# Optimization experiments

Measured on AMD Instinct MI355X. Metric: run time of the kernel, lower is better.

## Reference

```python
import jax, jax.numpy as jnp
import numpy as np

N_V = 100000   # vertices
N_E = 20000    # hyperedges
N_PAIRS = 1600000  # incidence pairs
F = 128
H = 128
EPS = 1e-5


def setup_inputs() -> dict:
    key = jax.random.key(0)
    k1, k2, k3, k4 = jax.random.split(key, 4)
    X = jax.random.normal(k1, (N_V, F), dtype=jnp.float32)
    vertex_ids = jax.random.randint(k2, (N_PAIRS,), 0, N_V, dtype=jnp.int32)
    edge_ids = jax.random.randint(k3, (N_PAIRS,), 0, N_E, dtype=jnp.int32)
    W = jax.random.normal(k4, (F, H), dtype=jnp.float32) * (1.0 / np.sqrt(F))
    b = jnp.zeros((H,), dtype=jnp.float32)
    gamma = jnp.ones((H,), dtype=jnp.float32)
    beta = jnp.zeros((H,), dtype=jnp.float32)
    return {"X": X, "vertex_ids": vertex_ids, "edge_ids": edge_ids,
            "W": W, "b": b, "gamma": gamma, "beta": beta}


def _segment_mean(vals, ids, num_segments):
    s = jax.ops.segment_sum(vals, ids, num_segments=num_segments)
    cnt = jax.ops.segment_sum(jnp.ones((ids.shape[0], 1), vals.dtype), ids,
                              num_segments=num_segments)
    return s / jnp.maximum(cnt, 1.0)


def reference(X, vertex_ids, edge_ids, W, b, gamma, beta):
    # linear: theta
    h = X @ W + b                                    # [N_V, H]
    # batchnorm (batch statistics, as in training mode)
    mu = jnp.mean(h, axis=0)
    var = jnp.var(h, axis=0)
    h = (h - mu) * jax.lax.rsqrt(var + EPS) * gamma + beta
    # hypergraph v2v mean: vertex -> hyperedge mean, then hyperedge -> vertex mean
    Xe = _segment_mean(h[vertex_ids], edge_ids, N_E)   # [N_E, H]
    Xv = _segment_mean(Xe[edge_ids], vertex_ids, N_V)  # [N_V, H]
    # activation (ReLU); dropout is identity in eval
    return jax.nn.relu(Xv)
```

## Files before the change

kernel.cpp:

```cpp
#include <hip/hip_runtime.h>
#include <hip/hip_bf16.h>

#define N_V 100000
#define N_E 20000
#define N_P 1600000
#define FDIM 128
#define HDIM 128
#define BN_EPS 1e-5f

#define SORT_C 4096
#define SORT_BLOCKS ((N_P + SORT_C - 1) / SORT_C)
#define NB_E 313
#define EB_SHIFT 6
#define EB_REGION 9216
#define EB_SORT 5888
#define NB_V 391
#define VB_SHIFT 8
#define VB_REGION 8192
#define VB_SORT 4608
#define SENTINEL 0xFFFFFFFFu

#define EIDX_CAP 192
#define VIDX_CAP 64

#define GEMM_BLOCKS 625
#define WT_STRIDE 136
#define BN_BLOCKS 400
#define BN_RPB 250

typedef __attribute__((ext_vector_type(8))) short short8;
typedef __attribute__((ext_vector_type(4))) float floatx4;

__device__ __forceinline__ float bf_lo(unsigned u) {
    return __uint_as_float(u << 16);
}
__device__ __forceinline__ float bf_hi(unsigned u) {
    return __uint_as_float(u & 0xffff0000u);
}
__device__ __forceinline__ unsigned short f2bf(float f) {
    unsigned u = __float_as_uint(f);
    return (unsigned short)((u + 0x7fffu + ((u >> 16) & 1u)) >> 16);
}

__device__ __forceinline__ void acc4(float* s, const uint2& u) {
    s[0] += bf_lo(u.x); s[1] += bf_hi(u.x);
    s[2] += bf_lo(u.y); s[3] += bf_hi(u.y);
}

__device__ __forceinline__ void acc8(float* s, const uint4& u) {
    s[0] += bf_lo(u.x); s[1] += bf_hi(u.x);
    s[2] += bf_lo(u.y); s[3] += bf_hi(u.y);
    s[4] += bf_lo(u.z); s[5] += bf_hi(u.z);
    s[6] += bf_lo(u.w); s[7] += bf_hi(u.w);
}

union SmemK1 {
    struct {
        unsigned short WTs[FDIM * WT_STRIDE];
    } g;
    struct {
        unsigned stage[SORT_C];
        int hist[NB_E], cur[NB_E], offs[NB_E], gbase[NB_E];
        int partial[256];
    } se;
    struct {
        unsigned stage[SORT_C];
        int hist[NB_V], cur[NB_V], offs[NB_V], gbase[NB_V];
        int partial[256];
    } sv;
};

union SmemBnCsr {
    struct {
        unsigned B[EB_SORT];
        int hist[256];
        int offs[257];
        int cur[256];
    } c;
    struct {
        float ls[128], lss[128];
    } b;
};

__device__ void gemm_body(int bid, unsigned short* WTs,
                          const float* __restrict__ X,
                          const float* __restrict__ W,
                          const float* __restrict__ bias,
                          unsigned* __restrict__ h_u) {
    const int t = threadIdx.x;
    for (int idx = t; idx < FDIM * HDIM; idx += 256) {
        const int k = idx >> 7, m = idx & 127;
        WTs[m * WT_STRIDE + k] = f2bf(W[idx]);
    }
    __syncthreads();

    const int wave = t >> 6, lane = t & 63;
    const int quad = lane >> 4, sub = lane & 15;
    const int nstrips = N_V / 16;

    for (int s = bid * 4 + wave; s < nstrips; s += GEMM_BLOCKS * 4) {
        const int row0 = s * 16;
        short8 xf[4];
        const float* xp = X + (size_t)(row0 + sub) * FDIM + quad * 8;
        #pragma unroll
        for (int kt = 0; kt < 4; ++kt) {
            const float4 a = *(const float4*)(xp + kt * 32);
            const float4 b2 = *(const float4*)(xp + kt * 32 + 4);
            short8 f;
            f[0] = (short)f2bf(a.x);  f[1] = (short)f2bf(a.y);
            f[2] = (short)f2bf(a.z);  f[3] = (short)f2bf(a.w);
            f[4] = (short)f2bf(b2.x); f[5] = (short)f2bf(b2.y);
            f[6] = (short)f2bf(b2.z); f[7] = (short)f2bf(b2.w);
            xf[kt] = f;
        }
        #pragma unroll
        for (int tile = 0; tile < 8; ++tile) {
            floatx4 acc = {0.f, 0.f, 0.f, 0.f};
            const unsigned short* wp =
                WTs + (tile * 16 + sub) * WT_STRIDE + quad * 8;
            #pragma unroll
            for (int kt = 0; kt < 4; ++kt) {
                const short8 af = *(const short8*)(wp + kt * 32);
                acc = __builtin_amdgcn_mfma_f32_16x16x32_bf16(af, xf[kt], acc,
                                                              0, 0, 0);
            }
            const int ch = tile * 16 + quad * 4;
            const float4 bb = *(const float4*)(bias + ch);
            const float c0 = acc[0] + bb.x, c1 = acc[1] + bb.y;
            const float c2 = acc[2] + bb.z, c3 = acc[3] + bb.w;
            const unsigned lo = (unsigned)f2bf(c0) | ((unsigned)f2bf(c1) << 16);
            const unsigned hi = (unsigned)f2bf(c2) | ((unsigned)f2bf(c3) << 16);
            uint2* dst = (uint2*)(h_u + (size_t)(row0 + sub) * 64 + (ch >> 1));
            *dst = make_uint2(lo, hi);
        }
    }
}

template <int NB, int BSHIFT, int REGION, bool EDGE>
__device__ void sort_dir_body(int bid, unsigned* stage, int* hist, int* cur,
                              int* offs, int* gbase, int* partial,
                              const int* __restrict__ keys,
                              const int* __restrict__ vals,
                              int* __restrict__ gcnt,
                              unsigned* __restrict__ part) {
    const int t = threadIdx.x;
    const int p0 = bid * SORT_C;
    const int n = min(SORT_C, N_P - p0);
    const int n4 = n >> 2;
    const int4* k4p = (const int4*)(keys + p0);
    const int4* v4p = (const int4*)(vals + p0);

    for (int k = t; k < NB; k += 256) hist[k] = 0;
    __syncthreads();
    for (int i = t; i < n4; i += 256) {
        const int4 k4 = k4p[i];
        atomicAdd(&hist[((unsigned)k4.x) >> BSHIFT], 1);
        atomicAdd(&hist[((unsigned)k4.y) >> BSHIFT], 1);
        atomicAdd(&hist[((unsigned)k4.z) >> BSHIFT], 1);
        atomicAdd(&hist[((unsigned)k4.w) >> BSHIFT], 1);
    }
    __syncthreads();
    {
        constexpr int G = (NB + 255) / 256;
        int loc[G]; int s = 0;
        #pragma unroll
        for (int g = 0; g < G; ++g) {
            int idx = t * G + g; loc[g] = s;
            if (idx < NB) s += hist[idx];
        }
        partial[t] = s;
        __syncthreads();
        for (int d = 1; d < 256; d <<= 1) {
            int x = (t >= d) ? partial[t - d] : 0;
            __syncthreads(); partial[t] += x; __syncthreads();
        }
        const int base = t ? partial[t - 1] : 0;
        #pragma unroll
        for (int g = 0; g < G; ++g) {
            int idx = t * G + g;
            if (idx < NB) { offs[idx] = base + loc[g]; cur[idx] = base + loc[g]; }
        }
        __syncthreads();
    }
    for (int i = t; i < n4; i += 256) {
        const int4 k4 = k4p[i];
        const int4 v4 = v4p[i];
        #pragma unroll
        for (int q = 0; q < 4; ++q) {
            const int kk = (q == 0) ? k4.x : (q == 1) ? k4.y : (q == 2) ? k4.z : k4.w;
            const int vv = (q == 0) ? v4.x : (q == 1) ? v4.y : (q == 2) ? v4.z : v4.w;
            const unsigned pk = EDGE
                ? (((unsigned)(kk & 63) << 17) | (unsigned)vv)
                : (((unsigned)(kk & 255) << 15) | (unsigned)vv);
            stage[atomicAdd(&cur[(unsigned)kk >> BSHIFT], 1)] = pk;
        }
    }
    __syncthreads();
    for (int k = t; k < NB; k += 256) {
        const int c = hist[k];
        gbase[k] = c ? atomicAdd(&gcnt[k], (c + 15) & ~15) : 0;
    }
    __syncthreads();
    for (int k = t >> 3; k < NB; k += 32) {
        const int c = hist[k];
        if (c == 0) continue;
        int cpad = (c + 15) & ~15;
        const int gb = gbase[k];
        if (gb >= REGION) continue;
        cpad = min(cpad, REGION - gb);
        unsigned* dst = part + (size_t)k * REGION + gb;
        const int lo = offs[k];
        for (int j = (t & 7) * 4; j + 3 < cpad; j += 32) {
            uint4 w;
            w.x = (j + 0 < c) ? stage[lo + j + 0] : SENTINEL;
            w.y = (j + 1 < c) ? stage[lo + j + 1] : SENTINEL;
            w.z = (j + 2 < c) ? stage[lo + j + 2] : SENTINEL;
            w.w = (j + 3 < c) ? stage[lo + j + 3] : SENTINEL;
            *(uint4*)(dst + j) = w;
        }
    }
}

__global__ __launch_bounds__(256) void k_gemm_sort(
    const float* __restrict__ X, const float* __restrict__ W,
    const float* __restrict__ bias, unsigned* __restrict__ h_u,
    const int* __restrict__ vid, const int* __restrict__ eid,
    int* __restrict__ gcntE, int* __restrict__ gcntV,
    unsigned* __restrict__ partE, unsigned* __restrict__ partV) {
    __shared__ __align__(16) SmemK1 sm;
    const int b = blockIdx.x;
    if (b < GEMM_BLOCKS) {
        gemm_body(b, sm.g.WTs, X, W, bias, h_u);
    } else if (b < GEMM_BLOCKS + SORT_BLOCKS) {
        sort_dir_body<NB_E, EB_SHIFT, EB_REGION, true>(
            b - GEMM_BLOCKS, sm.se.stage, sm.se.hist, sm.se.cur, sm.se.offs,
            sm.se.gbase, sm.se.partial, eid, vid, gcntE, partE);
    } else {
        sort_dir_body<NB_V, VB_SHIFT, VB_REGION, false>(
            b - GEMM_BLOCKS - SORT_BLOCKS, sm.sv.stage, sm.sv.hist, sm.sv.cur,
            sm.sv.offs, sm.sv.gbase, sm.sv.partial, vid, eid, gcntV, partV);
    }
}

__device__ void bn_body(int bid, float* ls, float* lss,
                        const unsigned* __restrict__ h_u,
                        float* __restrict__ sums) {
    const int t = threadIdx.x;
    const int c8 = t & 15;
    const int rw = t >> 4;
    const int r0 = bid * BN_RPB;
    const int r1 = min(r0 + BN_RPB, N_V);
    float s[8] = {0.f,0.f,0.f,0.f,0.f,0.f,0.f,0.f};
    float ss[8] = {0.f,0.f,0.f,0.f,0.f,0.f,0.f,0.f};
    for (int r = r0 + rw; r < r1; r += 16) {
        const uint4 u = *(const uint4*)(h_u + (size_t)r * 64 + c8 * 4);
        const float x0 = bf_lo(u.x), x1 = bf_hi(u.x);
        const float x2 = bf_lo(u.y), x3 = bf_hi(u.y);
        const float x4 = bf_lo(u.z), x5 = bf_hi(u.z);
        const float x6 = bf_lo(u.w), x7 = bf_hi(u.w);
        s[0]+=x0; ss[0]+=x0*x0;  s[1]+=x1; ss[1]+=x1*x1;
        s[2]+=x2; ss[2]+=x2*x2;  s[3]+=x3; ss[3]+=x3*x3;
        s[4]+=x4; ss[4]+=x4*x4;  s[5]+=x5; ss[5]+=x5*x5;
        s[6]+=x6; ss[6]+=x6*x6;  s[7]+=x7; ss[7]+=x7*x7;
    }
    #pragma unroll
    for (int k = 0; k < 8; ++k) {
        s[k]  += __shfl_xor(s[k], 16);  s[k]  += __shfl_xor(s[k], 32);
        ss[k] += __shfl_xor(ss[k], 16); ss[k] += __shfl_xor(ss[k], 32);
    }
    for (int k = t; k < 128; k += 256) { ls[k] = 0.f; lss[k] = 0.f; }
    __syncthreads();
    if ((t & 63) < 16) {
        #pragma unroll
        for (int k = 0; k < 8; ++k) {
            atomicAdd(&ls[c8 * 8 + k], s[k]);
            atomicAdd(&lss[c8 * 8 + k], ss[k]);
        }
    }
    __syncthreads();
    if (t < 128) {
        atomicAdd(&sums[t],       ls[t]);
        atomicAdd(&sums[128 + t], lss[t]);
    }
}

template <int NKEY, int PACK_SHIFT, int CAP, int REGION, int STRIDE>
__device__ void csr_body(int bkt, const unsigned* __restrict__ part,
                         const int* __restrict__ gcnt, int nkeys_total,
                         int* __restrict__ segoff, int* __restrict__ segcnt,
                         unsigned* __restrict__ csr,
                         unsigned* B, int* hist, int* offs, int* cur) {
    const int t = threadIdx.x;
    const unsigned mask = (1u << PACK_SHIFT) - 1u;
    const int tot = min(gcnt[bkt], REGION);
    const int tot4 = tot >> 2;
    const unsigned* src = part + (size_t)bkt * REGION;

    for (int k = t; k < NKEY; k += 256) { hist[k] = 0; cur[k] = 0; }
    __syncthreads();
    for (int i = t; i < tot4; i += 256) {
        const uint4 a = ((const uint4*)src)[i];
        if (a.x != SENTINEL) atomicAdd(&hist[a.x >> PACK_SHIFT], 1);
        if (a.y != SENTINEL) atomicAdd(&hist[a.y >> PACK_SHIFT], 1);
        if (a.z != SENTINEL) atomicAdd(&hist[a.z >> PACK_SHIFT], 1);
        if (a.w != SENTINEL) atomicAdd(&hist[a.w >> PACK_SHIFT], 1);
    }
    for (int i = tot4 * 4 + t; i < tot; i += 256) {
        const unsigned a = src[i];
        if (a != SENTINEL) atomicAdd(&hist[a >> PACK_SHIFT], 1);
    }
    __syncthreads();
    if (t == 0) {
        int acc = 0;
        for (int k = 0; k < NKEY; ++k) { offs[k] = acc; acc += hist[k]; }
        offs[NKEY] = acc;
    }
    __syncthreads();
    for (int i = t; i < tot4; i += 256) {
        const uint4 a = ((const uint4*)src)[i];
        #pragma unroll
        for (int q = 0; q < 4; ++q) {
            const unsigned av = (q == 0) ? a.x : (q == 1) ? a.y : (q == 2) ? a.z : a.w;
            if (av != SENTINEL) {
                const int k = av >> PACK_SHIFT;
                const int pos = offs[k] + atomicAdd(&cur[k], 1);
                if (pos < CAP) B[pos] = av & mask;
            }
        }
    }
    for (int i = tot4 * 4 + t; i < tot; i += 256) {
        const unsigned av = src[i];
        if (av != SENTINEL) {
            const int k = av >> PACK_SHIFT;
            const int pos = offs[k] + atomicAdd(&cur[k], 1);
            if (pos < CAP) B[pos] = av & mask;
        }
    }
    __syncthreads();
    const int total = min(offs[NKEY], CAP);
    unsigned* dst = csr + (size_t)bkt * STRIDE;
    for (int i = t * 4; i + 3 < total; i += 1024)
        *(uint4*)(dst + i) = *(const uint4*)(&B[i]);
    for (int i = (total & ~3) + t; i < total; i += 256) dst[i] = B[i];
    for (int k = t; k < NKEY; k += 256) {
        const int g = bkt * NKEY + k;
        if (g < nkeys_total) {
            const int o0 = min(offs[k], CAP);
            const int o1 = min(offs[k + 1], CAP);
            segoff[g] = bkt * STRIDE + o0;
            segcnt[g] = o1 - o0;
        }
    }
}

__global__ __launch_bounds__(256) void k_bn_csr(
    const unsigned* __restrict__ h_u, float* __restrict__ sums,
    const unsigned* __restrict__ partE, const int* __restrict__ gcntE,
    int* __restrict__ eoff, int* __restrict__ ecnt, unsigned* __restrict__ csrE,
    const unsigned* __restrict__ partV, const int* __restrict__ gcntV,
    int* __restrict__ voff, int* __restrict__ vcnt, unsigned* __restrict__ csrV) {
    __shared__ __align__(16) SmemBnCsr sm;
    const int b = blockIdx.x;
    if (b < BN_BLOCKS) {
        bn_body(b, sm.b.ls, sm.b.lss, h_u, sums);
    } else if (b < BN_BLOCKS + NB_E) {
        csr_body<64, 17, EB_SORT, EB_REGION, EB_SORT>(
            b - BN_BLOCKS, partE, gcntE, N_E, eoff, ecnt, csrE,
            sm.c.B, sm.c.hist, sm.c.offs, sm.c.cur);
    } else {
        csr_body<256, 15, VB_SORT, VB_REGION, VB_SORT>(
            b - BN_BLOCKS - NB_E, partV, gcntV, N_V, voff, vcnt, csrV,
            sm.c.B, sm.c.hist, sm.c.offs, sm.c.cur);
    }
}

__global__ __launch_bounds__(256) void k_edge_gather(
    const unsigned* __restrict__ h_u, const unsigned* __restrict__ csrE,
    const int* __restrict__ eoff, const int* __restrict__ ecnt,
    const float* __restrict__ sums, const float* __restrict__ gamma,
    const float* __restrict__ beta, unsigned* __restrict__ xe_u) {
    __shared__ int ib[4][EIDX_CAP];
    const int b = blockIdx.x;
    const int xcd = b & 7;
    const int half = xcd >> 2;
    const int grp = (b >> 3) * 4 + (xcd & 3);
    const int wave = threadIdx.x >> 6;
    const int e = grp * 4 + wave;
    const int l = threadIdx.x & 63;
    const int rg = l >> 4, c = l & 15;
    const int wbase = half * 32 + 2 * c;
    int o = 0, n = 0;
    if (e < N_E) { o = eoff[e]; n = ecnt[e]; }
    const int nc = min(n, EIDX_CAP);
    int* mi = ib[wave];
    for (int i = l; i < nc; i += 64) mi[i] = (int)csrE[o + i];
    __syncthreads();

    float s[4] = {0.f, 0.f, 0.f, 0.f};
    int j = 0;
    for (; j + 31 < nc; j += 32) {
        const int r0 = mi[j + rg],      r1 = mi[j + 4 + rg];
        const int r2 = mi[j + 8 + rg],  r3 = mi[j + 12 + rg];
        const int r4 = mi[j + 16 + rg], r5 = mi[j + 20 + rg];
        const int r6 = mi[j + 24 + rg], r7 = mi[j + 28 + rg];
        const uint2 u0 = *(const uint2*)(h_u + (size_t)r0 * 64 + wbase);
        const uint2 u1 = *(const uint2*)(h_u + (size_t)r1 * 64 + wbase);
        const uint2 u2 = *(const uint2*)(h_u + (size_t)r2 * 64 + wbase);
        const uint2 u3 = *(const uint2*)(h_u + (size_t)r3 * 64 + wbase);
        const uint2 u4 = *(const uint2*)(h_u + (size_t)r4 * 64 + wbase);
        const uint2 u5 = *(const uint2*)(h_u + (size_t)r5 * 64 + wbase);
        const uint2 u6 = *(const uint2*)(h_u + (size_t)r6 * 64 + wbase);
        const uint2 u7 = *(const uint2*)(h_u + (size_t)r7 * 64 + wbase);
        acc4(s, u0); acc4(s, u1); acc4(s, u2); acc4(s, u3);
        acc4(s, u4); acc4(s, u5); acc4(s, u6); acc4(s, u7);
    }
    for (; j + 15 < nc; j += 16) {
        const int r0 = mi[j + rg],     r1 = mi[j + 4 + rg];
        const int r2 = mi[j + 8 + rg], r3 = mi[j + 12 + rg];
        const uint2 u0 = *(const uint2*)(h_u + (size_t)r0 * 64 + wbase);
        const uint2 u1 = *(const uint2*)(h_u + (size_t)r1 * 64 + wbase);
        const uint2 u2 = *(const uint2*)(h_u + (size_t)r2 * 64 + wbase);
        const uint2 u3 = *(const uint2*)(h_u + (size_t)r3 * 64 + wbase);
        acc4(s, u0); acc4(s, u1); acc4(s, u2); acc4(s, u3);
    }
    for (; j < nc; j += 4) {
        if (j + rg < nc) {
            const int r = mi[j + rg];
            const uint2 u = *(const uint2*)(h_u + (size_t)r * 64 + wbase);
            acc4(s, u);
        }
    }
    for (int jj = nc; jj < n; jj += 4) {
        if (jj + rg < n) {
            const int r = (int)csrE[o + jj + rg];
            const uint2 u = *(const uint2*)(h_u + (size_t)r * 64 + wbase);
            acc4(s, u);
        }
    }
    #pragma unroll
    for (int k = 0; k < 4; ++k) {
        s[k] += __shfl_xor(s[k], 16);
        s[k] += __shfl_xor(s[k], 32);
    }
    if (e < N_E && rg == 0) {
        const float inv_n = 1.0f / (float)N_V;
        const float rc = (n > 0) ? (1.0f / (float)n) : 0.f;
        float m[4];
        #pragma unroll
        for (int q = 0; q < 4; ++q) {
            const int ch = half * 64 + c * 4 + q;
            float mv = 0.f;
            if (n > 0) {
                const float mu  = sums[ch] * inv_n;
                const float var = sums[128 + ch] * inv_n - mu * mu;
                const float inv = rsqrtf(var + BN_EPS);
                const float sc  = gamma[ch] * inv;
                const float sh  = beta[ch] - mu * sc;
                mv = sc * s[q] * rc + sh;
            }
            m[q] = mv;
        }
        uint2 pk;
        pk.x = (unsigned)f2bf(m[0]) | ((unsigned)f2bf(m[1]) << 16);
        pk.y = (unsigned)f2bf(m[2]) | ((unsigned)f2bf(m[3]) << 16);
        *(uint2*)(xe_u + (size_t)e * 64 + wbase) = pk;
    }
}

__global__ __launch_bounds__(256) void k_vert_gather(
    const unsigned* __restrict__ xe_u, const unsigned* __restrict__ csrV,
    const int* __restrict__ voff, const int* __restrict__ vcnt,
    float* __restrict__ out) {
    __shared__ int ib[4][VIDX_CAP];
    const int wave = threadIdx.x >> 6;
    const int v = blockIdx.x * 4 + wave;
    const int l = threadIdx.x & 63;
    const int g = l >> 4, c = l & 15;
    int o = 0, n = 0;
    if (v < N_V) { o = voff[v]; n = vcnt[v]; }
    const int nc = min(n, VIDX_CAP);
    int* mi = ib[wave];
    for (int i = l; i < nc; i += 64) mi[i] = (int)csrV[o + i];
    __syncthreads();

    float s[8] = {0.f, 0.f, 0.f, 0.f, 0.f, 0.f, 0.f, 0.f};
    int j = 0;
    for (; j + 15 < nc; j += 16) {
        const int r0 = mi[j + g],     r1 = mi[j + 4 + g];
        const int r2 = mi[j + 8 + g], r3 = mi[j + 12 + g];
        const uint4 u0 = *(const uint4*)(xe_u + (size_t)r0 * 64 + 4 * c);
        const uint4 u1 = *(const uint4*)(xe_u + (size_t)r1 * 64 + 4 * c);
        const uint4 u2 = *(const uint4*)(xe_u + (size_t)r2 * 64 + 4 * c);
        const uint4 u3 = *(const uint4*)(xe_u + (size_t)r3 * 64 + 4 * c);
        acc8(s, u0); acc8(s, u1); acc8(s, u2); acc8(s, u3);
    }
    for (; j < nc; j += 4) {
        if (j + g < nc) {
            const int r = mi[j + g];
            const uint4 u = *(const uint4*)(xe_u + (size_t)r * 64 + 4 * c);
            acc8(s, u);
        }
    }
    for (int jj = nc; jj < n; jj += 4) {
        if (jj + g < n) {
            const int r = (int)csrV[o + jj + g];
            const uint4 u = *(const uint4*)(xe_u + (size_t)r * 64 + 4 * c);
            acc8(s, u);
        }
    }
    #pragma unroll
    for (int k = 0; k < 8; ++k) {
        s[k] += __shfl_xor(s[k], 16);
        s[k] += __shfl_xor(s[k], 32);
    }
    if (v < N_V && g == 0) {
        const float rc = 1.0f / (float)max(n, 1);
        float4 r0, r1;
        r0.x = fmaxf(s[0] * rc, 0.f);
        r0.y = fmaxf(s[1] * rc, 0.f);
        r0.z = fmaxf(s[2] * rc, 0.f);
        r0.w = fmaxf(s[3] * rc, 0.f);
        r1.x = fmaxf(s[4] * rc, 0.f);
        r1.y = fmaxf(s[5] * rc, 0.f);
        r1.z = fmaxf(s[6] * rc, 0.f);
        r1.w = fmaxf(s[7] * rc, 0.f);
        ((float4*)out)[(size_t)v * 32 + 2 * c]     = r0;
        ((float4*)out)[(size_t)v * 32 + 2 * c + 1] = r1;
    }
}

extern "C" void kernel_launch(void* const* d_in, const int* in_sizes, int n_in,
                              void* d_out, int out_size, void* d_ws, size_t ws_size,
                              hipStream_t stream) {
    const float* X     = (const float*)d_in[0];
    const int*   vid   = (const int*)d_in[1];
    const int*   eid   = (const int*)d_in[2];
    const float* W     = (const float*)d_in[3];
    const float* b     = (const float*)d_in[4];
    const float* gamma = (const float*)d_in[5];
    const float* beta  = (const float*)d_in[6];
    float* out = (float*)d_out;

    char* ws = (char*)d_ws;
    unsigned* h_u   = (unsigned*)ws;  ws += (size_t)N_V * 64 * 4;
    unsigned* xe_u  = (unsigned*)ws;  ws += (size_t)N_E * 64 * 4;
    unsigned* partE = (unsigned*)ws;  ws += (size_t)NB_E * EB_REGION * 4;
    unsigned* partV = (unsigned*)ws;  ws += (size_t)NB_V * VB_REGION * 4;
    unsigned* csrE  = (unsigned*)ws;  ws += (size_t)NB_E * EB_SORT * 4;
    unsigned* csrV  = (unsigned*)ws;  ws += (size_t)NB_V * VB_SORT * 4;
    int* eoff = (int*)ws;             ws += (size_t)N_E * 4;
    int* ecnt = (int*)ws;             ws += (size_t)N_E * 4;
    int* voff = (int*)ws;             ws += (size_t)N_V * 4;
    int* vcnt = (int*)ws;             ws += (size_t)N_V * 4;
    char* zbase = ws;
    int*   gcntE = (int*)ws;          ws += (size_t)NB_E * 4;
    int*   gcntV = (int*)ws;          ws += (size_t)NB_V * 4;
    float* sums  = (float*)ws;        ws += 256 * 4;
    char* zend = ws;

    hipMemsetAsync(zbase, 0, (size_t)(zend - zbase), stream);

    k_gemm_sort<<<GEMM_BLOCKS + 2 * SORT_BLOCKS, 256, 0, stream>>>(
        X, W, b, h_u, vid, eid, gcntE, gcntV, partE, partV);

    k_bn_csr<<<BN_BLOCKS + NB_E + NB_V, 256, 0, stream>>>(
        h_u, sums, partE, gcntE, eoff, ecnt, csrE,
        partV, gcntV, voff, vcnt, csrV);

    k_edge_gather<<<(N_E / 4) * 2, 256, 0, stream>>>(h_u, csrE, eoff, ecnt,
                                                     sums, gamma, beta, xe_u);
    k_vert_gather<<<(N_V + 3) / 4, 256, 0, stream>>>(xe_u, csrV, voff, vcnt,
                                                     out);
}
```

Measured before the change: 262.0 us.

## Move vertex CSR build into edge-gather kernel and parallelize bucket prefix scan

```diff
diff --git a/kernel.cpp b/kernel.cpp
--- a/kernel.cpp
+++ b/kernel.cpp
@@ -27,6 +27,8 @@
 #define WT_STRIDE 136
 #define BN_BLOCKS 400
 #define BN_RPB 250
+
+#define CSRV_BLOCKS 392
 
 typedef __attribute__((ext_vector_type(8))) short short8;
 typedef __attribute__((ext_vector_type(4))) float floatx4;
@@ -70,16 +72,30 @@
     } sv;
 };
 
-union SmemBnCsr {
+union SmemBnCsrE {
     struct {
         unsigned B[EB_SORT];
-        int hist[256];
-        int offs[257];
-        int cur[256];
+        int hist[64];
+        int offs[65];
+        int cur[64];
+        int partial[256];
     } c;
     struct {
         float ls[128], lss[128];
     } b;
+};
+
+union SmemEdgeCsrV {
+    struct {
+        unsigned B[VB_SORT];
+        int hist[256];
+        int offs[257];
+        int cur[256];
+        int partial[256];
+    } c;
+    struct {
+        int ib[4][EIDX_CAP];
+    } e;
 };
 
 __device__ void gemm_body(int bid, unsigned short* WTs,
@@ -289,7 +305,8 @@
                          const int* __restrict__ gcnt, int nkeys_total,
                          int* __restrict__ segoff, int* __restrict__ segcnt,
                          unsigned* __restrict__ csr,
-                         unsigned* B, int* hist, int* offs, int* cur) {
+                         unsigned* B, int* hist, int* offs, int* cur,
+                         int* partial) {
     const int t = threadIdx.x;
     const unsigned mask = (1u << PACK_SHIFT) - 1u;
     const int tot = min(gcnt[bkt], REGION);
@@ -310,12 +327,18 @@
         if (a != SENTINEL) atomicAdd(&hist[a >> PACK_SHIFT], 1);
     }
     __syncthreads();
-    if (t == 0) {
-        int acc = 0;
-        for (int k = 0; k < NKEY; ++k) { offs[k] = acc; acc += hist[k]; }
-        offs[NKEY] = acc;
-    }
-    __syncthreads();
+    {
+        const int h = (t < NKEY) ? hist[t] : 0;
+        partial[t] = h;
+        __syncthreads();
+        for (int d = 1; d < 256; d <<= 1) {
+            int x = (t >= d) ? partial[t - d] : 0;
+            __syncthreads(); partial[t] += x; __syncthreads();
+        }
+        if (t < NKEY) offs[t] = partial[t] - h;
+        if (t == NKEY - 1) offs[NKEY] = partial[t];
+        __syncthreads();
+    }
     for (int i = t; i < tot4; i += 256) {
         const uint4 a = ((const uint4*)src)[i];
         #pragma unroll
@@ -353,34 +376,30 @@
     }
 }
 
-__global__ __launch_bounds__(256) void k_bn_csr(
+__global__ __launch_bounds__(256) void k_bn_csre(
     const unsigned* __restrict__ h_u, float* __restrict__ sums,
     const unsigned* __restrict__ partE, const int* __restrict__ gcntE,
-    int* __restrict__ eoff, int* __restrict__ ecnt, unsigned* __restrict__ csrE,
-    const unsigned* __restrict__ partV, const int* __restrict__ gcntV,
-    int* __restrict__ voff, int* __restrict__ vcnt, unsigned* __restrict__ csrV) {
-    __shared__ __align__(16) SmemBnCsr sm;
+    int* __restrict__ eoff, int* __restrict__ ecnt, unsigned* __restrict__ csrE) {
+    __shared__ __align__(16) SmemBnCsrE sm;
     const int b = blockIdx.x;
     if (b < BN_BLOCKS) {
         bn_body(b, sm.b.ls, sm.b.lss, h_u, sums);
-    } else if (b < BN_BLOCKS + NB_E) {
+    } else {
         csr_body<64, 17, EB_SORT, EB_REGION, EB_SORT>(
             b - BN_BLOCKS, partE, gcntE, N_E, eoff, ecnt, csrE,
-            sm.c.B, sm.c.hist, sm.c.offs, sm.c.cur);
-    } else {
-        csr_body<256, 15, VB_SORT, VB_REGION, VB_SORT>(
-            b - BN_BLOCKS - NB_E, partV, gcntV, N_V, voff, vcnt, csrV,
-            sm.c.B, sm.c.hist, sm.c.offs, sm.c.cur);
-    }
-}
-
-__global__ __launch_bounds__(256) void k_edge_gather(
-    const unsigned* __restrict__ h_u, const unsigned* __restrict__ csrE,
-    const int* __restrict__ eoff, const int* __restrict__ ecnt,
-    const float* __restrict__ sums, const float* __restrict__ gamma,
-    const float* __restrict__ beta, unsigned* __restrict__ xe_u) {
-    __shared__ int ib[4][EIDX_CAP];
-    const int b = blockIdx.x;
+            sm.c.B, sm.c.hist, sm.c.offs, sm.c.cur, sm.c.partial);
+    }
+}
+
+__device__ void edge_body(int b, int* ib ,
+                          const unsigned* __restrict__ h_u,
+                          const unsigned* __restrict__ csrE,
+                          const int* __restrict__ eoff,
+                          const int* __restrict__ ecnt,
+                          const float* __restrict__ sums,
+                          const float* __restrict__ gamma,
+                          const float* __restrict__ beta,
+                          unsigned* __restrict__ xe_u) {
     const int xcd = b & 7;
     const int half = xcd >> 2;
     const int grp = (b >> 3) * 4 + (xcd & 3);
@@ -392,7 +411,7 @@
     int o = 0, n = 0;
     if (e < N_E) { o = eoff[e]; n = ecnt[e]; }
     const int nc = min(n, EIDX_CAP);
-    int* mi = ib[wave];
+    int* mi = ib + wave * EIDX_CAP;
     for (int i = l; i < nc; i += 64) mi[i] = (int)csrE[o + i];
     __syncthreads();
 
@@ -467,6 +486,26 @@
     }
 }
 
+__global__ __launch_bounds__(256) void k_edge_csrv(
+    const unsigned* __restrict__ h_u, const unsigned* __restrict__ csrE,
+    const int* __restrict__ eoff, const int* __restrict__ ecnt,
+    const float* __restrict__ sums, const float* __restrict__ gamma,
+    const float* __restrict__ beta, unsigned* __restrict__ xe_u,
+    const unsigned* __restrict__ partV, const int* __restrict__ gcntV,
+    int* __restrict__ voff, int* __restrict__ vcnt, unsigned* __restrict__ csrV) {
+    __shared__ __align__(16) SmemEdgeCsrV sm;
+    const int b = blockIdx.x;
+    if (b < CSRV_BLOCKS) {
+        if (b >= NB_V) return;
+        csr_body<256, 15, VB_SORT, VB_REGION, VB_SORT>(
+            b, partV, gcntV, N_V, voff, vcnt, csrV,
+            sm.c.B, sm.c.hist, sm.c.offs, sm.c.cur, sm.c.partial);
+    } else {
+        edge_body(b - CSRV_BLOCKS, &sm.e.ib[0][0], h_u, csrE, eoff, ecnt,
+                  sums, gamma, beta, xe_u);
+    }
+}
+
 __global__ __launch_bounds__(256) void k_vert_gather(
     const unsigned* __restrict__ xe_u, const unsigned* __restrict__ csrV,
     const int* __restrict__ voff, const int* __restrict__ vcnt,
@@ -563,12 +602,13 @@
     k_gemm_sort<<<GEMM_BLOCKS + 2 * SORT_BLOCKS, 256, 0, stream>>>(
         X, W, b, h_u, vid, eid, gcntE, gcntV, partE, partV);
 
-    k_bn_csr<<<BN_BLOCKS + NB_E + NB_V, 256, 0, stream>>>(
-        h_u, sums, partE, gcntE, eoff, ecnt, csrE,
+    k_bn_csre<<<BN_BLOCKS + NB_E, 256, 0, stream>>>(
+        h_u, sums, partE, gcntE, eoff, ecnt, csrE);
+
+    k_edge_csrv<<<CSRV_BLOCKS + (N_E / 4) * 2, 256, 0, stream>>>(
+        h_u, csrE, eoff, ecnt, sums, gamma, beta, xe_u,
         partV, gcntV, voff, vcnt, csrV);
 
-    k_edge_gather<<<(N_E / 4) * 2, 256, 0, stream>>>(h_u, csrE, eoff, ecnt,
-                                                     sums, gamma, beta, xe_u);
     k_vert_gather<<<(N_V + 3) / 4, 256, 0, stream>>>(xe_u, csrV, voff, vcnt,
                                                      out);
 }
```

After: 268.8 us. 2.6% more time.
